# Performance work log

Measured on AMD Instinct MI355X. Metric: run time of the kernel, lower is better.

The kernel has to match this reference:

```python
import jax, jax.numpy as jnp
import numpy as np

D_IN = 256
D_OUT = 256
N0, N1, N2 = 200000, 40000, 8000
E1, E2 = 1000000, 200000


def setup_inputs() -> dict:
    key = jax.random.key(0)
    ks = jax.random.split(key, 12)
    s = 1.0 / np.sqrt(D_IN)
    nodes = jax.random.normal(ks[0], (N0, D_IN), dtype=jnp.float32)
    W_l1 = jax.random.normal(ks[1], (D_OUT, D_IN), dtype=jnp.float32) * s
    b1 = jnp.zeros((D_OUT,), dtype=jnp.float32)
    W_r1 = jax.random.normal(ks[2], (D_OUT, D_IN), dtype=jnp.float32) * s
    W_l2 = jax.random.normal(ks[3], (D_OUT, D_OUT), dtype=jnp.float32) * s
    b2 = jnp.zeros((D_OUT,), dtype=jnp.float32)
    W_r2 = jax.random.normal(ks[4], (D_OUT, D_OUT), dtype=jnp.float32) * s
    src1 = jax.random.randint(ks[5], (E1,), 0, N0, dtype=jnp.int32)
    dst1 = jax.random.randint(ks[6], (E1,), 0, N1, dtype=jnp.int32)
    src2 = jax.random.randint(ks[7], (E2,), 0, N1, dtype=jnp.int32)
    dst2 = jax.random.randint(ks[8], (E2,), 0, N2, dtype=jnp.int32)
    return {"nodes": nodes, "W_l1": W_l1, "b1": b1, "W_r1": W_r1,
            "W_l2": W_l2, "b2": b2, "W_r2": W_r2,
            "src1": src1, "dst1": dst1, "src2": src2, "dst2": dst2,
            "n1": N1, "n2": N2}


def _sage_layer(x, src, dst, n_tgt, Wl, b, Wr):
    # PyG SAGEConv (mean aggr, bipartite): lin_l(mean_j x_src[j]) + lin_r(x_tgt)
    x_tgt = x[:n_tgt]
    agg = jax.ops.segment_sum(x[src], dst, num_segments=n_tgt)  # [n_tgt, d]
    cnt = jax.ops.segment_sum(jnp.ones(src.shape, dtype=x.dtype), dst,
                              num_segments=n_tgt)
    mean = agg / jnp.maximum(cnt, 1.0)[:, None]
    out = mean @ Wl.T + b + x_tgt @ Wr.T
    return jnp.tanh(out)  # tanh applied by _GraphSAGE.forward


def reference(nodes, W_l1, b1, W_r1, W_l2, b2, W_r2, src1, dst1, src2, dst2, n1, n2):
    h = _sage_layer(nodes, src1, dst1, n1, W_l1, b1, W_r1)  # [n1, D_OUT]
    h = _sage_layer(h, src2, dst2, n2, W_l2, b2, W_r2)      # [n2, D_OUT]
    return h
```

## Files before the change

### kernel.cpp

```cpp
#include <hip/hip_runtime.h>
#include <math.h>

#define D 256
#define KK 512
#define NC1 40
#define NC2 8

typedef __attribute__((ext_vector_type(8))) short short8;
typedef __attribute__((ext_vector_type(4))) float f32x4;

__device__ __forceinline__ unsigned short f2bf(float f) {
    unsigned u = __builtin_bit_cast(unsigned, f);
    u += 0x7fffu + ((u >> 16) & 1u);
    return (unsigned short)(u >> 16);
}
__device__ __forceinline__ float bf2f(unsigned short h) {
    unsigned u = ((unsigned)h) << 16;
    return __builtin_bit_cast(float, u);
}
__device__ __forceinline__ float tanh_fast(float x) {
    return 1.0f - 2.0f / (__expf(2.0f * x) + 1.0f);
}

__global__ __launch_bounds__(256) void hist_kernel(const int* __restrict__ dst1, int E1,
                                                   const int* __restrict__ dst2, int E2,
                                                   int* cnt1, int* cnt2) {
    int t = blockIdx.x * 256 + threadIdx.x;
    if (t < E1) {
        atomicAdd(&cnt1[dst1[t]], 1);
    } else if (t < E1 + E2) {
        atomicAdd(&cnt2[dst2[t - E1]], 1);
    }
}

__global__ __launch_bounds__(256) void scan_phase1(const int* __restrict__ cnt1, int n1, int* off1, int* part1,
                                                   const int* __restrict__ cnt2, int n2, int* off2, int* part2) {
    int b = blockIdx.x;
    const int* cnt; int n; int* off; int* part; int c;
    if (b < NC1) { cnt = cnt1; n = n1; off = off1; part = part1; c = b; }
    else         { cnt = cnt2; n = n2; off = off2; part = part2; c = b - NC1; }
    int t = threadIdx.x;
    int i0 = c * 1024 + t * 4;
    int v[4];
#pragma unroll
    for (int j = 0; j < 4; ++j) v[j] = (i0 + j < n) ? cnt[i0 + j] : 0;
    int s = v[0] + v[1] + v[2] + v[3];
    int lane = t & 63, wid = t >> 6;
    int ps = s;
#pragma unroll
    for (int d = 1; d < 64; d <<= 1) {
        int tmp = __shfl_up(ps, d);
        if (lane >= d) ps += tmp;
    }
    __shared__ int wsum[4];
    if (lane == 63) wsum[wid] = ps;
    __syncthreads();
    int wbase = 0;
    for (int k = 0; k < wid; ++k) wbase += wsum[k];
    int run = wbase + ps - s;
#pragma unroll
    for (int j = 0; j < 4; ++j) {
        if (i0 + j < n) off[i0 + j] = run;
        run += v[j];
    }
    if (t == 255) part[c] = wbase + ps;
}

__global__ __launch_bounds__(64) void scan_phase2(int* part1, int* part2) {
    if (threadIdx.x == 0) {
        int s = 0;
        for (int i = 0; i < NC1; ++i) { int v = part1[i]; part1[i] = s; s += v; }
        part1[NC1] = s;
    } else if (threadIdx.x == 1) {
        int s = 0;
        for (int i = 0; i < NC2; ++i) { int v = part2[i]; part2[i] = s; s += v; }
        part2[NC2] = s;
    }
}

__global__ __launch_bounds__(256) void scan_phase3(int* off1, int n1, const int* __restrict__ part1,
                                                   int* off2, int n2, const int* __restrict__ part2) {
    int b = blockIdx.x;
    int n; int* off; const int* part; int c;
    if (b < NC1) { n = n1; off = off1; part = part1; c = b; }
    else         { n = n2; off = off2; part = part2; c = b - NC1; }
    int t = threadIdx.x;
    int i0 = c * 1024 + t * 4;
    int add = part[c];
#pragma unroll
    for (int j = 0; j < 4; ++j)
        if (i0 + j < n) off[i0 + j] += add;
    if (b == 0 && t == 0) off1[n1] = part1[NC1];
    if (b == NC1 && t == 0) off2[n2] = part2[NC2];
}

__global__ __launch_bounds__(256) void prep_kernel(const int* __restrict__ off1, const int* __restrict__ cnt1,
                                                   int* cur1, float* recip1, int n1,
                                                   const int* __restrict__ off2, const int* __restrict__ cnt2,
                                                   int* cur2, float* recip2, int n2) {
    int t = blockIdx.x * 256 + threadIdx.x;
    if (t < n1) {
        cur1[t] = off1[t];
        recip1[t] = 1.0f / fmaxf((float)cnt1[t], 1.0f);
    } else if (t < n1 + n2) {
        int u = t - n1;
        cur2[u] = off2[u];
        recip2[u] = 1.0f / fmaxf((float)cnt2[u], 1.0f);
    }
}

__global__ __launch_bounds__(256) void sort_kernel(const int* __restrict__ src1, const int* __restrict__ dst1, int E1,
                                                   int* cur1, int* sorted1,
                                                   const int* __restrict__ src2, const int* __restrict__ dst2, int E2,
                                                   int* cur2, int* sorted2) {
    int t = blockIdx.x * 256 + threadIdx.x;
    if (t < E1) {
        int d = dst1[t];
        int p = atomicAdd(&cur1[d], 1);
        sorted1[p] = src1[t];
    } else if (t < E1 + E2) {
        int u = t - E1;
        int d = dst2[u];
        int p = atomicAdd(&cur2[d], 1);
        sorted2[p] = src2[u];
    }
}

__global__ __launch_bounds__(256) void prep_weights(const float* __restrict__ Wl1, const float* __restrict__ Wr1,
                                                    const float* __restrict__ Wl2, const float* __restrict__ Wr2,
                                                    unsigned short* Wc1, unsigned short* Wc2) {
    int t = blockIdx.x * 256 + threadIdx.x;
    int which = t >> 17;
    int u = t & 131071;
    int nrow = u >> 9;
    int k = u & 511;
    const float* Wl = which ? Wl2 : Wl1;
    const float* Wr = which ? Wr2 : Wr1;
    unsigned short* Wc = which ? Wc2 : Wc1;
    float v = (k < 256) ? Wl[nrow * 256 + k] : Wr[nrow * 256 + (k - 256)];
    Wc[u] = f2bf(v);
}

__global__ __launch_bounds__(256) void aggregate_f32(const float* __restrict__ x,
                                                     const int* __restrict__ sorted,
                                                     const int* __restrict__ off,
                                                     const float* __restrict__ recip,
                                                     unsigned short* __restrict__ mean, int n) {
    int node = blockIdx.x * 4 + (threadIdx.x >> 6);
    if (node >= n) return;
    int l = threadIdx.x & 63;
    int beg = off[node], end = off[node + 1];

    float4 a0 = {0.f, 0.f, 0.f, 0.f};
    float4 a1 = {0.f, 0.f, 0.f, 0.f};
    int e = beg;
    for (; e + 1 < end; e += 2) {
        int s0 = sorted[e];
        int s1 = sorted[e + 1];
        float4 v0 = *(const float4*)(x + (size_t)s0 * D + l * 4);
        float4 v1 = *(const float4*)(x + (size_t)s1 * D + l * 4);
        a0.x += v0.x; a0.y += v0.y; a0.z += v0.z; a0.w += v0.w;
        a1.x += v1.x; a1.y += v1.y; a1.z += v1.z; a1.w += v1.w;
    }
    if (e < end) {
        int s = sorted[e];
        float4 v = *(const float4*)(x + (size_t)s * D + l * 4);
        a0.x += v.x; a0.y += v.y; a0.z += v.z; a0.w += v.w;
    }
    float r = recip[node];
    ushort4 o;
    o.x = f2bf((a0.x + a1.x) * r);
    o.y = f2bf((a0.y + a1.y) * r);
    o.z = f2bf((a0.z + a1.z) * r);
    o.w = f2bf((a0.w + a1.w) * r);
    *(ushort4*)(mean + (size_t)node * D + l * 4) = o;
}

__global__ __launch_bounds__(256) void aggregate_bf16(const unsigned short* __restrict__ x,
                                                      const int* __restrict__ sorted,
                                                      const int* __restrict__ off,
                                                      const float* __restrict__ recip,
                                                      unsigned short* __restrict__ mean, int n) {
    int node = blockIdx.x * 4 + (threadIdx.x >> 6);
    if (node >= n) return;
    int l = threadIdx.x & 63;
    int beg = off[node], end = off[node + 1];

    float a[4] = {0.f, 0.f, 0.f, 0.f};
    for (int e = beg; e < end; ++e) {
        int s = sorted[e];
        ushort4 v = *(const ushort4*)(x + (size_t)s * D + l * 4);
        a[0] += bf2f(v.x); a[1] += bf2f(v.y); a[2] += bf2f(v.z); a[3] += bf2f(v.w);
    }
    float r = recip[node];
    ushort4 o;
    o.x = f2bf(a[0] * r);
    o.y = f2bf(a[1] * r);
    o.z = f2bf(a[2] * r);
    o.w = f2bf(a[3] * r);
    *(ushort4*)(mean + (size_t)node * D + l * 4) = o;
}

template<bool X_FP32, bool OUT_BF16>
__global__ __launch_bounds__(256) void sage_gemm_mfma(const unsigned short* __restrict__ meanp,
                                                      const void* __restrict__ xp,
                                                      const unsigned short* __restrict__ Wcat,
                                                      const float* __restrict__ bias,
                                                      void* __restrict__ outp,
                                                      int M) {
    __shared__ unsigned short Asb[128 * 72];
    __shared__ unsigned short Wsb[128 * 72];

    const int tid = threadIdx.x;
    const int lane = tid & 63;
    const int w = tid >> 6;
    const int wm = w & 1, wn = w >> 1;
    const int quad = lane >> 4, lr = lane & 15;
    const int row0 = blockIdx.x * 128;
    const int n0 = blockIdx.y * 128;

    f32x4 acc[4][4] = {};

    for (int kt = 0; kt < 8; ++kt) {
        const bool mh = (kt < 4);
        const int kg0 = mh ? kt * 64 : (kt - 4) * 64;

#pragma unroll
        for (int i = 0; i < 4; ++i) {
            int f = i * 256 + tid;
            int r = f >> 3;
            int c8 = (f & 7) * 8;
            int gr = row0 + r;
            unsigned short tmp[8];
            if (gr < M) {
                if (mh) {
                    *(short8*)tmp = *(const short8*)(meanp + (size_t)gr * D + kg0 + c8);
                } else if (X_FP32) {
                    const float* xf = (const float*)xp + (size_t)gr * D + kg0 + c8;
                    float4 v0 = *(const float4*)xf;
                    float4 v1 = *(const float4*)(xf + 4);
                    tmp[0] = f2bf(v0.x); tmp[1] = f2bf(v0.y); tmp[2] = f2bf(v0.z); tmp[3] = f2bf(v0.w);
                    tmp[4] = f2bf(v1.x); tmp[5] = f2bf(v1.y); tmp[6] = f2bf(v1.z); tmp[7] = f2bf(v1.w);
                } else {
                    *(short8*)tmp = *(const short8*)((const unsigned short*)xp + (size_t)gr * D + kg0 + c8);
                }
            } else {
#pragma unroll
                for (int j = 0; j < 8; ++j) tmp[j] = 0;
            }
            *(short8*)&Asb[r * 72 + c8] = *(short8*)tmp;
        }

#pragma unroll
        for (int i = 0; i < 4; ++i) {
            int f = i * 256 + tid;
            int nn = f >> 3;
            int c8 = (f & 7) * 8;
            *(short8*)&Wsb[nn * 72 + c8] =
                *(const short8*)(Wcat + (size_t)(n0 + nn) * KK + kt * 64 + c8);
        }

        __syncthreads();

#pragma unroll
        for (int ks = 0; ks < 64; ks += 32) {
            short8 a[4], b[4];
#pragma unroll
            for (int mt = 0; mt < 4; ++mt)
                a[mt] = *(const short8*)&Asb[(wm * 64 + mt * 16 + lr) * 72 + ks + quad * 8];
#pragma unroll
            for (int nt = 0; nt < 4; ++nt)
                b[nt] = *(const short8*)&Wsb[(wn * 64 + nt * 16 + lr) * 72 + ks + quad * 8];
#pragma unroll
            for (int mt = 0; mt < 4; ++mt)
#pragma unroll
                for (int nt = 0; nt < 4; ++nt)
                    acc[mt][nt] = __builtin_amdgcn_mfma_f32_16x16x32_bf16(a[mt], b[nt], acc[mt][nt], 0, 0, 0);
        }

        __syncthreads();
    }

#pragma unroll
    for (int mt = 0; mt < 4; ++mt) {
        int gr0 = row0 + wm * 64 + mt * 16 + quad * 4;
#pragma unroll
        for (int nt = 0; nt < 4; ++nt) {
            int col = n0 + wn * 64 + nt * 16 + lr;
            float bc = bias[col];
#pragma unroll
            for (int r = 0; r < 4; ++r) {
                int gr = gr0 + r;
                if (gr < M) {
                    float v = tanh_fast(acc[mt][nt][r] + bc);
                    if (OUT_BF16) ((unsigned short*)outp)[(size_t)gr * D + col] = f2bf(v);
                    else          ((float*)outp)[(size_t)gr * D + col] = v;
                }
            }
        }
    }
}

extern "C" void kernel_launch(void* const* d_in, const int* in_sizes, int n_in,
                              void* d_out, int out_size, void* d_ws, size_t ws_size,
                              hipStream_t stream) {
    const float* nodes = (const float*)d_in[0];
    const float* W_l1  = (const float*)d_in[1];
    const float* b1    = (const float*)d_in[2];
    const float* W_r1  = (const float*)d_in[3];
    const float* W_l2  = (const float*)d_in[4];
    const float* b2    = (const float*)d_in[5];
    const float* W_r2  = (const float*)d_in[6];
    const int* src1 = (const int*)d_in[7];
    const int* dst1 = (const int*)d_in[8];
    const int* src2 = (const int*)d_in[9];
    const int* dst2 = (const int*)d_in[10];

    const int E1 = in_sizes[7];
    const int E2 = in_sizes[9];
    const int N1 = 40000;
    const int N2 = 8000;

    char* p = (char*)d_ws;
    auto carve = [&](size_t bytes) -> char* {
        char* q = p;
        p += (bytes + 255) & ~(size_t)255;
        return q;
    };
    unsigned short* mean1 = (unsigned short*)carve((size_t)N1 * D * 2);
    unsigned short* h1    = (unsigned short*)carve((size_t)N1 * D * 2);
    unsigned short* mean2 = (unsigned short*)carve((size_t)N2 * D * 2);
    unsigned short* Wc1   = (unsigned short*)carve((size_t)D * KK * 2);
    unsigned short* Wc2   = (unsigned short*)carve((size_t)D * KK * 2);
    float* recip1 = (float*)carve((size_t)N1 * 4);
    float* recip2 = (float*)carve((size_t)N2 * 4);
    int* cnt1 = (int*)carve((size_t)(N1 + N2) * 4);
    int* cnt2 = cnt1 + N1;
    int* off1 = (int*)carve((size_t)(N1 + 1) * 4);
    int* off2 = (int*)carve((size_t)(N2 + 1) * 4);
    int* cur1 = (int*)carve((size_t)N1 * 4);
    int* cur2 = (int*)carve((size_t)N2 * 4);
    int* part1 = (int*)carve((size_t)(NC1 + 1) * 4);
    int* part2 = (int*)carve((size_t)(NC2 + 1) * 4);
    int* sorted1 = (int*)carve((size_t)E1 * 4);
    int* sorted2 = (int*)carve((size_t)E2 * 4);

    hipMemsetAsync(cnt1, 0, (size_t)(N1 + N2) * sizeof(int), stream);

    int totE = E1 + E2;
    hist_kernel<<<(totE + 255) / 256, 256, 0, stream>>>(dst1, E1, dst2, E2, cnt1, cnt2);
    scan_phase1<<<NC1 + NC2, 256, 0, stream>>>(cnt1, N1, off1, part1, cnt2, N2, off2, part2);
    scan_phase2<<<1, 64, 0, stream>>>(part1, part2);
    scan_phase3<<<NC1 + NC2, 256, 0, stream>>>(off1, N1, part1, off2, N2, part2);
    {
        int totN = N1 + N2;
        prep_kernel<<<(totN + 255) / 256, 256, 0, stream>>>(off1, cnt1, cur1, recip1, N1,
                                                            off2, cnt2, cur2, recip2, N2);
    }
    sort_kernel<<<(totE + 255) / 256, 256, 0, stream>>>(src1, dst1, E1, cur1, sorted1,
                                                        src2, dst2, E2, cur2, sorted2);
    prep_weights<<<1024, 256, 0, stream>>>(W_l1, W_r1, W_l2, W_r2, Wc1, Wc2);

    aggregate_f32<<<N1 / 4, 256, 0, stream>>>(nodes, sorted1, off1, recip1, mean1, N1);
    sage_gemm_mfma<true, true><<<dim3((N1 + 127) / 128, 2), 256, 0, stream>>>(
        mean1, (const void*)nodes, Wc1, b1, (void*)h1, N1);

    aggregate_bf16<<<N2 / 4, 256, 0, stream>>>(h1, sorted2, off2, recip2, mean2, N2);
    sage_gemm_mfma<false, false><<<dim3((N2 + 127) / 128, 2), 256, 0, stream>>>(
        mean2, (const void*)h1, Wc2, b2, d_out, N2);
}
```

Baseline: 632.6 us.

## Pre-convert input nodes to bf16 and unroll bf16 gather-aggregation by four

Adds a pass that converts the whole fp32 node feature matrix to bf16 in workspace. Layer-1 aggregation and the GEMM then read the bf16 copy, halving the bytes moved by the random row gathers. The bf16 aggregation loop is also unrolled by four with independent accumulators to keep more loads in flight. The conversion reads all 200k fp32 rows and writes a 100MB buffer, even though only gathered rows and the first 40k are needed. That cost may offset the gather savings, and the path falls back to fp32 if the workspace is too small.

New measurement: 617.0 us. 2.5% less time.

```diff
diff --git a/kernel.cpp b/kernel.cpp
--- a/kernel.cpp
+++ b/kernel.cpp
@@ -20,6 +20,19 @@
 }
 __device__ __forceinline__ float tanh_fast(float x) {
     return 1.0f - 2.0f / (__expf(2.0f * x) + 1.0f);
+}
+
+__global__ __launch_bounds__(256) void convert_nodes(const float* __restrict__ x,
+                                                     unsigned short* __restrict__ y, int total8) {
+    int t = blockIdx.x * 256 + threadIdx.x;
+    if (t >= total8) return;
+    const float* xp = x + (size_t)t * 8;
+    float4 v0 = *(const float4*)xp;
+    float4 v1 = *(const float4*)(xp + 4);
+    unsigned short o[8];
+    o[0] = f2bf(v0.x); o[1] = f2bf(v0.y); o[2] = f2bf(v0.z); o[3] = f2bf(v0.w);
+    o[4] = f2bf(v1.x); o[5] = f2bf(v1.y); o[6] = f2bf(v1.z); o[7] = f2bf(v1.w);
+    *(short8*)(y + (size_t)t * 8) = *(short8*)o;
 }
 
 __global__ __launch_bounds__(256) void hist_kernel(const int* __restrict__ dst1, int E1,
@@ -186,18 +199,33 @@
     int l = threadIdx.x & 63;
     int beg = off[node], end = off[node + 1];
 
-    float a[4] = {0.f, 0.f, 0.f, 0.f};
-    for (int e = beg; e < end; ++e) {
+    float a0[4] = {0.f, 0.f, 0.f, 0.f};
+    float a1[4] = {0.f, 0.f, 0.f, 0.f};
+    float a2[4] = {0.f, 0.f, 0.f, 0.f};
+    float a3[4] = {0.f, 0.f, 0.f, 0.f};
+    int e = beg;
+    for (; e + 3 < end; e += 4) {
+        int s0 = sorted[e], s1 = sorted[e + 1], s2 = sorted[e + 2], s3 = sorted[e + 3];
+        ushort4 v0 = *(const ushort4*)(x + (size_t)s0 * D + l * 4);
+        ushort4 v1 = *(const ushort4*)(x + (size_t)s1 * D + l * 4);
+        ushort4 v2 = *(const ushort4*)(x + (size_t)s2 * D + l * 4);
+        ushort4 v3 = *(const ushort4*)(x + (size_t)s3 * D + l * 4);
+        a0[0] += bf2f(v0.x); a0[1] += bf2f(v0.y); a0[2] += bf2f(v0.z); a0[3] += bf2f(v0.w);
+        a1[0] += bf2f(v1.x); a1[1] += bf2f(v1.y); a1[2] += bf2f(v1.z); a1[3] += bf2f(v1.w);
+        a2[0] += bf2f(v2.x); a2[1] += bf2f(v2.y); a2[2] += bf2f(v2.z); a2[3] += bf2f(v2.w);
+        a3[0] += bf2f(v3.x); a3[1] += bf2f(v3.y); a3[2] += bf2f(v3.z); a3[3] += bf2f(v3.w);
+    }
+    for (; e < end; ++e) {
         int s = sorted[e];
         ushort4 v = *(const ushort4*)(x + (size_t)s * D + l * 4);
-        a[0] += bf2f(v.x); a[1] += bf2f(v.y); a[2] += bf2f(v.z); a[3] += bf2f(v.w);
+        a0[0] += bf2f(v.x); a0[1] += bf2f(v.y); a0[2] += bf2f(v.z); a0[3] += bf2f(v.w);
     }
     float r = recip[node];
     ushort4 o;
-    o.x = f2bf(a[0] * r);
-    o.y = f2bf(a[1] * r);
-    o.z = f2bf(a[2] * r);
-    o.w = f2bf(a[3] * r);
+    o.x = f2bf((a0[0] + a1[0] + a2[0] + a3[0]) * r);
+    o.y = f2bf((a0[1] + a1[1] + a2[1] + a3[1]) * r);
+    o.z = f2bf((a0[2] + a1[2] + a2[2] + a3[2]) * r);
+    o.w = f2bf((a0[3] + a1[3] + a2[3] + a3[3]) * r);
     *(ushort4*)(mean + (size_t)node * D + l * 4) = o;
 }
 
@@ -318,6 +346,7 @@
 
     const int E1 = in_sizes[7];
     const int E2 = in_sizes[9];
+    const int N0 = in_sizes[0] / D;
     const int N1 = 40000;
     const int N2 = 8000;
 
@@ -344,6 +373,8 @@
     int* part2 = (int*)carve((size_t)(NC2 + 1) * 4);
     int* sorted1 = (int*)carve((size_t)E1 * 4);
     int* sorted2 = (int*)carve((size_t)E2 * 4);
+    unsigned short* nodes_bf = (unsigned short*)carve((size_t)N0 * D * 2);
+    const bool use_bf = ((size_t)(p - (char*)d_ws) <= ws_size);
 
     hipMemsetAsync(cnt1, 0, (size_t)(N1 + N2) * sizeof(int), stream);
 
@@ -361,9 +392,18 @@
                                                         src2, dst2, E2, cur2, sorted2);
     prep_weights<<<1024, 256, 0, stream>>>(W_l1, W_r1, W_l2, W_r2, Wc1, Wc2);
 
-    aggregate_f32<<<N1 / 4, 256, 0, stream>>>(nodes, sorted1, off1, recip1, mean1, N1);
-    sage_gemm_mfma<true, true><<<dim3((N1 + 127) / 128, 2), 256, 0, stream>>>(
-        mean1, (const void*)nodes, Wc1, b1, (void*)h1, N1);
+    if (use_bf) {
+        int total8 = N0 * D / 8;
+        convert_nodes<<<(total8 + 255) / 256, 256, 0, stream>>>(nodes, nodes_bf, total8);
+
+        aggregate_bf16<<<N1 / 4, 256, 0, stream>>>(nodes_bf, sorted1, off1, recip1, mean1, N1);
+        sage_gemm_mfma<false, true><<<dim3((N1 + 127) / 128, 2), 256, 0, stream>>>(
+            mean1, (const void*)nodes_bf, Wc1, b1, (void*)h1, N1);
+    } else {
+        aggregate_f32<<<N1 / 4, 256, 0, stream>>>(nodes, sorted1, off1, recip1, mean1, N1);
+        sage_gemm_mfma<true, true><<<dim3((N1 + 127) / 128, 2), 256, 0, stream>>>(
+            mean1, (const void*)nodes, Wc1, b1, (void*)h1, N1);
+    }
 
     aggregate_bf16<<<N2 / 4, 256, 0, stream>>>(h1, sorted2, off2, recip2, mean2, N2);
     sage_gemm_mfma<false, false><<<dim3((N2 + 127) / 128, 2), 256, 0, stream>>>(
```

## Pre-convert node features to bf16 and fuse prologue kernels

Applied to the files above, without the earlier changes.

Adds a prologue kernel that converts all node features to bf16 while also doing the degree histogram and weight packing, and merges the scan fix-up with the cur/recip prep. Layer-1 aggregation and GEMM then read bf16 node rows instead of fp32, halving the gather traffic. The bf16 aggregation is rewritten to use 16-byte loads with two edges per wavefront and four accumulators for more memory-level parallelism. The trade-off is a full extra read and write pass over the 200k x 256 feature matrix, plus extra workspace; it falls back to the fp32 path if the workspace is too small.

Result: faster. 598.3 us (-5.4%).

```diff
diff --git a/kernel.cpp b/kernel.cpp
--- a/kernel.cpp
+++ b/kernel.cpp
@@ -22,14 +22,44 @@
     return 1.0f - 2.0f / (__expf(2.0f * x) + 1.0f);
 }
 
-__global__ __launch_bounds__(256) void hist_kernel(const int* __restrict__ dst1, int E1,
-                                                   const int* __restrict__ dst2, int E2,
-                                                   int* cnt1, int* cnt2) {
-    int t = blockIdx.x * 256 + threadIdx.x;
-    if (t < E1) {
-        atomicAdd(&cnt1[dst1[t]], 1);
-    } else if (t < E1 + E2) {
-        atomicAdd(&cnt2[dst2[t - E1]], 1);
+__global__ __launch_bounds__(256) void prologue(const float* __restrict__ nodes,
+                                                unsigned short* __restrict__ nodes_bf, int total8, int CB,
+                                                const int* __restrict__ dst1, int E1,
+                                                const int* __restrict__ dst2, int E2,
+                                                int* cnt1, int* cnt2, int HB,
+                                                const float* __restrict__ Wl1, const float* __restrict__ Wr1,
+                                                const float* __restrict__ Wl2, const float* __restrict__ Wr2,
+                                                unsigned short* Wc1, unsigned short* Wc2) {
+    int b = blockIdx.x;
+    if (b < CB) {
+        int t = b * 256 + threadIdx.x;
+        if (t < total8) {
+            const float* xp = nodes + (size_t)t * 8;
+            float4 v0 = *(const float4*)xp;
+            float4 v1 = *(const float4*)(xp + 4);
+            unsigned short o[8];
+            o[0] = f2bf(v0.x); o[1] = f2bf(v0.y); o[2] = f2bf(v0.z); o[3] = f2bf(v0.w);
+            o[4] = f2bf(v1.x); o[5] = f2bf(v1.y); o[6] = f2bf(v1.z); o[7] = f2bf(v1.w);
+            *(short8*)(nodes_bf + (size_t)t * 8) = *(short8*)o;
+        }
+    } else if (b < CB + HB) {
+        int t = (b - CB) * 256 + threadIdx.x;
+        if (t < E1) {
+            atomicAdd(&cnt1[dst1[t]], 1);
+        } else if (t < E1 + E2) {
+            atomicAdd(&cnt2[dst2[t - E1]], 1);
+        }
+    } else {
+        int t = (b - CB - HB) * 256 + threadIdx.x;
+        int which = t >> 17;
+        int u = t & 131071;
+        int nrow = u >> 9;
+        int k = u & 511;
+        const float* Wl = which ? Wl2 : Wl1;
+        const float* Wr = which ? Wr2 : Wr1;
+        unsigned short* Wc = which ? Wc2 : Wc1;
+        float v = (k < 256) ? Wl[nrow * 256 + k] : Wr[nrow * 256 + (k - 256)];
+        Wc[u] = f2bf(v);
     }
 }
 
@@ -78,35 +108,29 @@
     }
 }
 
-__global__ __launch_bounds__(256) void scan_phase3(int* off1, int n1, const int* __restrict__ part1,
-                                                   int* off2, int n2, const int* __restrict__ part2) {
+__global__ __launch_bounds__(256) void scan_phase3_prep(int* off1, const int* __restrict__ cnt1,
+                                                        int* cur1, float* recip1, int n1, const int* __restrict__ part1,
+                                                        int* off2, const int* __restrict__ cnt2,
+                                                        int* cur2, float* recip2, int n2, const int* __restrict__ part2) {
     int b = blockIdx.x;
-    int n; int* off; const int* part; int c;
-    if (b < NC1) { n = n1; off = off1; part = part1; c = b; }
-    else         { n = n2; off = off2; part = part2; c = b - NC1; }
+    int n; int* off; const int* part; const int* cnt; int* cur; float* recip; int c;
+    if (b < NC1) { n = n1; off = off1; part = part1; cnt = cnt1; cur = cur1; recip = recip1; c = b; }
+    else         { n = n2; off = off2; part = part2; cnt = cnt2; cur = cur2; recip = recip2; c = b - NC1; }
     int t = threadIdx.x;
     int i0 = c * 1024 + t * 4;
     int add = part[c];
 #pragma unroll
-    for (int j = 0; j < 4; ++j)
-        if (i0 + j < n) off[i0 + j] += add;
+    for (int j = 0; j < 4; ++j) {
+        int i = i0 + j;
+        if (i < n) {
+            int v = off[i] + add;
+            off[i] = v;
+            cur[i] = v;
+            recip[i] = 1.0f / fmaxf((float)cnt[i], 1.0f);
+        }
+    }
     if (b == 0 && t == 0) off1[n1] = part1[NC1];
     if (b == NC1 && t == 0) off2[n2] = part2[NC2];
-}
-
-__global__ __launch_bounds__(256) void prep_kernel(const int* __restrict__ off1, const int* __restrict__ cnt1,
-                                                   int* cur1, float* recip1, int n1,
-                                                   const int* __restrict__ off2, const int* __restrict__ cnt2,
-                                                   int* cur2, float* recip2, int n2) {
-    int t = blockIdx.x * 256 + threadIdx.x;
-    if (t < n1) {
-        cur1[t] = off1[t];
-        recip1[t] = 1.0f / fmaxf((float)cnt1[t], 1.0f);
-    } else if (t < n1 + n2) {
-        int u = t - n1;
-        cur2[u] = off2[u];
-        recip2[u] = 1.0f / fmaxf((float)cnt2[u], 1.0f);
-    }
 }
 
 __global__ __launch_bounds__(256) void sort_kernel(const int* __restrict__ src1, const int* __restrict__ dst1, int E1,
@@ -126,21 +150,6 @@
     }
 }
 
-__global__ __launch_bounds__(256) void prep_weights(const float* __restrict__ Wl1, const float* __restrict__ Wr1,
-                                                    const float* __restrict__ Wl2, const float* __restrict__ Wr2,
-                                                    unsigned short* Wc1, unsigned short* Wc2) {
-    int t = blockIdx.x * 256 + threadIdx.x;
-    int which = t >> 17;
-    int u = t & 131071;
-    int nrow = u >> 9;
-    int k = u & 511;
-    const float* Wl = which ? Wl2 : Wl1;
-    const float* Wr = which ? Wr2 : Wr1;
-    unsigned short* Wc = which ? Wc2 : Wc1;
-    float v = (k < 256) ? Wl[nrow * 256 + k] : Wr[nrow * 256 + (k - 256)];
-    Wc[u] = f2bf(v);
-}
-
 __global__ __launch_bounds__(256) void aggregate_f32(const float* __restrict__ x,
                                                      const int* __restrict__ sorted,
                                                      const int* __restrict__ off,
@@ -184,21 +193,48 @@
     int node = blockIdx.x * 4 + (threadIdx.x >> 6);
     if (node >= n) return;
     int l = threadIdx.x & 63;
+    int slot = l >> 5;
+    int li = l & 31;
     int beg = off[node], end = off[node + 1];
 
-    float a[4] = {0.f, 0.f, 0.f, 0.f};
-    for (int e = beg; e < end; ++e) {
-        int s = sorted[e];
-        ushort4 v = *(const ushort4*)(x + (size_t)s * D + l * 4);
-        a[0] += bf2f(v.x); a[1] += bf2f(v.y); a[2] += bf2f(v.z); a[3] += bf2f(v.w);
+    float a0[8] = {}, a1[8] = {}, a2[8] = {}, a3[8] = {};
+    int e = beg;
+    for (; e + 7 < end; e += 8) {
+        int s0 = sorted[e + slot];
+        int s1 = sorted[e + 2 + slot];
+        int s2 = sorted[e + 4 + slot];
+        int s3 = sorted[e + 6 + slot];
+        short8 v0 = *(const short8*)(x + (size_t)s0 * D + li * 8);
+        short8 v1 = *(const short8*)(x + (size_t)s1 * D + li * 8);
+        short8 v2 = *(const short8*)(x + (size_t)s2 * D + li * 8);
+        short8 v3 = *(const short8*)(x + (size_t)s3 * D + li * 8);
+#pragma unroll
+        for (int k = 0; k < 8; ++k) {
+            a0[k] += bf2f((unsigned short)v0[k]);
+            a1[k] += bf2f((unsigned short)v1[k]);
+            a2[k] += bf2f((unsigned short)v2[k]);
+            a3[k] += bf2f((unsigned short)v3[k]);
+        }
+    }
+    for (; e < end; e += 2) {
+        int me = e + slot;
+        if (me < end) {
+            int s = sorted[me];
+            short8 v = *(const short8*)(x + (size_t)s * D + li * 8);
+#pragma unroll
+            for (int k = 0; k < 8; ++k) a0[k] += bf2f((unsigned short)v[k]);
+        }
     }
     float r = recip[node];
-    ushort4 o;
-    o.x = f2bf(a[0] * r);
-    o.y = f2bf(a[1] * r);
-    o.z = f2bf(a[2] * r);
-    o.w = f2bf(a[3] * r);
-    *(ushort4*)(mean + (size_t)node * D + l * 4) = o;
+    unsigned short o[8];
+#pragma unroll
+    for (int k = 0; k < 8; ++k) {
+        float t = a0[k] + a1[k] + a2[k] + a3[k];
+        t += __shfl_xor(t, 32);
+        o[k] = f2bf(t * r);
+    }
+    if (slot == 0)
+        *(short8*)(mean + (size_t)node * D + li * 8) = *(short8*)o;
 }
 
 template<bool X_FP32, bool OUT_BF16>
@@ -318,6 +354,7 @@
 
     const int E1 = in_sizes[7];
     const int E2 = in_sizes[9];
+    const int N0 = in_sizes[0] / D;
     const int N1 = 40000;
     const int N2 = 8000;
 
@@ -344,26 +381,36 @@
     int* part2 = (int*)carve((size_t)(NC2 + 1) * 4);
     int* sorted1 = (int*)carve((size_t)E1 * 4);
     int* sorted2 = (int*)carve((size_t)E2 * 4);
+    unsigned short* nodes_bf = (unsigned short*)carve((size_t)N0 * D * 2);
+    const bool use_bf = ((size_t)(p - (char*)d_ws) <= ws_size);
 
     hipMemsetAsync(cnt1, 0, (size_t)(N1 + N2) * sizeof(int), stream);
 
-    int totE = E1 + E2;
-    hist_kernel<<<(totE + 255) / 256, 256, 0, stream>>>(dst1, E1, dst2, E2, cnt1, cnt2);
+    const int totE = E1 + E2;
+    const int total8 = N0 * D / 8;
+    const int CB = use_bf ? (total8 + 255) / 256 : 0;
+    const int HB = (totE + 255) / 256;
+    const int WB = (2 * D * KK + 255) / 256;
+
+    prologue<<<CB + HB + WB, 256, 0, stream>>>(nodes, nodes_bf, total8, CB,
+                                               dst1, E1, dst2, E2, cnt1, cnt2, HB,
+                                               W_l1, W_r1, W_l2, W_r2, Wc1, Wc2);
     scan_phase1<<<NC1 + NC2, 256, 0, stream>>>(cnt1, N1, off1, part1, cnt2, N2, off2, part2);
     scan_phase2<<<1, 64, 0, stream>>>(part1, part2);
-    scan_phase3<<<NC1 + NC2, 256, 0, stream>>>(off1, N1, part1, off2, N2, part2);
-    {
-        int totN = N1 + N2;
-        prep_kernel<<<(totN + 255) / 256, 256, 0, stream>>>(off1, cnt1, cur1, recip1, N1,
-                                                            off2, cnt2, cur2, recip2, N2);
-    }
+    scan_phase3_prep<<<NC1 + NC2, 256, 0, stream>>>(off1, cnt1, cur1, recip1, N1, part1,
+                                                    off2, cnt2, cur2, recip2, N2, part2);
     sort_kernel<<<(totE + 255) / 256, 256, 0, stream>>>(src1, dst1, E1, cur1, sorted1,
                                                         src2, dst2, E2, cur2, sorted2);
-    prep_weights<<<1024, 256, 0, stream>>>(W_l1, W_r1, W_l2, W_r2, Wc1, Wc2);
-
-    aggregate_f32<<<N1 / 4, 256, 0, stream>>>(nodes, sorted1, off1, recip1, mean1, N1);
-    sage_gemm_mfma<true, true><<<dim3((N1 + 127) / 128, 2), 256, 0, stream>>>(
-        mean1, (const void*)nodes, Wc1, b1, (void*)h1, N1);
+
+    if (use_bf) {
+        aggregate_bf16<<<N1 / 4, 256, 0, stream>>>(nodes_bf, sorted1, off1, recip1, mean1, N1);
+        sage_gemm_mfma<false, true><<<dim3((N1 + 127) / 128, 2), 256, 0, stream>>>(
+            mean1, (const void*)nodes_bf, Wc1, b1, (void*)h1, N1);
+    } else {
+        aggregate_f32<<<N1 / 4, 256, 0, stream>>>(nodes, sorted1, off1, recip1, mean1, N1);
+        sage_gemm_mfma<true, true><<<dim3((N1 + 127) / 128, 2), 256, 0, stream>>>(
+            mean1, (const void*)nodes, Wc1, b1, (void*)h1, N1);
+    }
 
     aggregate_bf16<<<N2 / 4, 256, 0, stream>>>(h1, sorted2, off2, recip2, mean2, N2);
     sage_gemm_mfma<false, false><<<dim3((N2 + 127) / 128, 2), 256, 0, stream>>>(
```
